# Kernel tuning notes

Measured on AMD Instinct MI355X. Metric: run time of the kernel, lower is better.

## Reference

```python
import jax, jax.numpy as jnp
import numpy as np
from jax import lax

N, CIN, COUT = 4, 3, 16
D = H = W = 64
K, S, PAD, OUT_PAD = 3, 2, 1, 1


def setup_inputs() -> dict:
    key = jax.random.key(0)
    k1, k2, k3, k4 = jax.random.split(key, 4)
    x = jax.random.normal(k1, (N, CIN, D, H, W), dtype=jnp.float32)
    # torch ConvTranspose3d weight layout: [Cin, Cout, kD, kH, kW]
    w = jax.random.normal(k2, (CIN, COUT, K, K, K), dtype=jnp.float32) * 0.1
    b = jax.random.normal(k3, (COUT,), dtype=jnp.float32) * 0.1
    subtract = jax.random.normal(k4, (COUT,), dtype=jnp.float32) * 0.1
    return {"x": x, "w": w, "b": b, "subtract": subtract}


def reference(x, w, b, subtract):
    # ConvTranspose3d(k=3, s=2, p=1, output_padding=1) as a dilated conv:
    # flip kernel spatially, swap in/out channel axes, lhs_dilation = stride,
    # padding low = k-1-p = 1, padding high = k-1-p+output_padding = 2.
    w_conv = jnp.flip(jnp.transpose(w, (1, 0, 2, 3, 4)), axis=(2, 3, 4))  # [Cout,Cin,k,k,k]
    y = lax.conv_general_dilated(
        x, w_conv,
        window_strides=(1, 1, 1),
        padding=[(1, 2), (1, 2), (1, 2)],
        lhs_dilation=(S, S, S),
        dimension_numbers=("NCDHW", "OIDHW", "NCDHW"),
    )  # [N, 16, 2D, 2H, 2W]
    y = y + b[None, :, None, None, None]
    # MaxPool3d(kernel=2, stride=2, pad=0)
    y = lax.reduce_window(
        y, -jnp.inf, lax.max,
        window_dimensions=(1, 1, 2, 2, 2),
        window_strides=(1, 1, 2, 2, 2),
        padding="VALID",
    )  # [N, 16, D, H, W]
    s = jax.nn.softmax(y, axis=1)                       # channel softmax
    z = s - subtract[None, :, None, None, None]          # per-channel subtract
    sw = z * jax.nn.sigmoid(z)                           # swish
    return jnp.max(sw, axis=1)                           # max over channels -> [N, D, H, W]
```

## Files before the change

### kernel.cpp

```cpp
#include <hip/hip_runtime.h>
#include <math.h>

#define CIN   3
#define COUT  16
#define DHW   64

__global__ __launch_bounds__(256) void fused_convt_pool_softmax_swish_max(
    const float* __restrict__ x,
    const float* __restrict__ w,
    const float* __restrict__ bias,
    const float* __restrict__ sub,
    float* __restrict__ out)
{
    const int wv = threadIdx.x;
    const int h  = blockIdx.x * blockDim.y + threadIdx.y;
    const int d  = blockIdx.y;
    const int n  = blockIdx.z;

    float xr[CIN][2][2][2];
    const size_t nbase = (size_t)n * CIN * DHW * DHW * DHW;
#pragma unroll
    for (int c = 0; c < CIN; ++c) {
#pragma unroll
        for (int dd = 0; dd < 2; ++dd) {
#pragma unroll
            for (int hh = 0; hh < 2; ++hh) {
                const int id = d + dd;
                const int ih = h + hh;
                float v = 0.0f;
                if (id < DHW && ih < DHW) {
                    v = x[nbase + (((size_t)c * DHW + id) * DHW + ih) * DHW + wv];
                }
                xr[c][dd][hh][0] = v;
                float v1 = __shfl_down(v, 1, 64);
                xr[c][dd][hh][1] = (wv == 63) ? 0.0f : v1;
            }
        }
    }

    float pooled[COUT];
#pragma unroll
    for (int co = 0; co < COUT; ++co) {
        float acc[2][2][2] = {{{0.0f,0.0f},{0.0f,0.0f}},{{0.0f,0.0f},{0.0f,0.0f}}};
#pragma unroll
        for (int c = 0; c < CIN; ++c) {
            const float* wp = w + ((size_t)c * COUT + co) * 27;
#pragma unroll
            for (int kd = 0; kd < 3; ++kd) {
                const int pd = (kd == 1) ? 0 : 1;
                const int dd = (kd == 0) ? 1 : 0;
#pragma unroll
                for (int kh = 0; kh < 3; ++kh) {
                    const int ph = (kh == 1) ? 0 : 1;
                    const int hh = (kh == 0) ? 1 : 0;
#pragma unroll
                    for (int kw = 0; kw < 3; ++kw) {
                        const int pw = (kw == 1) ? 0 : 1;
                        const int ww = (kw == 0) ? 1 : 0;
                        acc[pd][ph][pw] = fmaf(wp[kd * 9 + kh * 3 + kw],
                                               xr[c][dd][hh][ww],
                                               acc[pd][ph][pw]);
                    }
                }
            }
        }
        float mx = acc[0][0][0];
        mx = fmaxf(mx, acc[0][0][1]);
        mx = fmaxf(mx, acc[0][1][0]);
        mx = fmaxf(mx, acc[0][1][1]);
        mx = fmaxf(mx, acc[1][0][0]);
        mx = fmaxf(mx, acc[1][0][1]);
        mx = fmaxf(mx, acc[1][1][0]);
        mx = fmaxf(mx, acc[1][1][1]);
        pooled[co] = mx + bias[co];
    }

    float m = pooled[0];
#pragma unroll
    for (int co = 1; co < COUT; ++co) m = fmaxf(m, pooled[co]);
    float e[COUT];
    float s = 0.0f;
#pragma unroll
    for (int co = 0; co < COUT; ++co) {
        e[co] = __expf(pooled[co] - m);
        s += e[co];
    }
    const float inv = 1.0f / s;

    float best = -3.402823466e+38f;
#pragma unroll
    for (int co = 0; co < COUT; ++co) {
        const float z  = fmaf(e[co], inv, -sub[co]);
        const float sw = z / (1.0f + __expf(-z));
        best = fmaxf(best, sw);
    }

    out[(((size_t)n * DHW + d) * DHW + h) * DHW + wv] = best;
}

extern "C" void kernel_launch(void* const* d_in, const int* in_sizes, int n_in,
                              void* d_out, int out_size, void* d_ws, size_t ws_size,
                              hipStream_t stream) {
    const float* x   = (const float*)d_in[0];
    const float* w   = (const float*)d_in[1];
    const float* b   = (const float*)d_in[2];
    const float* sub = (const float*)d_in[3];
    float* out = (float*)d_out;

    dim3 block(64, 4, 1);
    dim3 grid(DHW / 4, DHW, 4);
    fused_convt_pool_softmax_swish_max<<<grid, block, 0, stream>>>(x, w, b, sub, out);
}
```

Measured before the change: 113.9 us.

## Compute two W outputs per thread with vectorized loads and fast reciprocals

Each thread now handles two adjacent output columns. It loads a float2 plus one neighbour from each input row in place of using a cross-lane shuffle, so every weight load is reused for twice the FMAs and the stores become float2. The block shape changes to 32x8, and launch bounds add a minimum-occupancy hint. Division in the softmax and sigmoid is replaced by hardware reciprocal approximations, which trades a little precision for fewer instructions. Register pressure roughly doubles, since there are twice as many accumulators and pooled values, which could lower occupancy or cause spills.

New measurement: 107.7 us. 5.4% less time.

```diff
diff --git a/kernel.cpp b/kernel.cpp
--- a/kernel.cpp
+++ b/kernel.cpp
@@ -5,19 +5,20 @@
 #define COUT  16
 #define DHW   64
 
-__global__ __launch_bounds__(256) void fused_convt_pool_softmax_swish_max(
+__global__ __launch_bounds__(256, 4) void fused_convt_pool_softmax_swish_max(
     const float* __restrict__ x,
     const float* __restrict__ w,
     const float* __restrict__ bias,
     const float* __restrict__ sub,
     float* __restrict__ out)
 {
-    const int wv = threadIdx.x;
+    const int tp = threadIdx.x;
     const int h  = blockIdx.x * blockDim.y + threadIdx.y;
     const int d  = blockIdx.y;
     const int n  = blockIdx.z;
+    const int w0 = tp * 2;
 
-    float xr[CIN][2][2][2];
+    float xr[CIN][2][2][3];
     const size_t nbase = (size_t)n * CIN * DHW * DHW * DHW;
 #pragma unroll
     for (int c = 0; c < CIN; ++c) {
@@ -27,24 +28,37 @@
             for (int hh = 0; hh < 2; ++hh) {
                 const int id = d + dd;
                 const int ih = h + hh;
-                float v = 0.0f;
+                float v0 = 0.0f, v1 = 0.0f, v2 = 0.0f;
                 if (id < DHW && ih < DHW) {
-                    v = x[nbase + (((size_t)c * DHW + id) * DHW + ih) * DHW + wv];
+                    const float* row = x + nbase + (((size_t)c * DHW + id) * DHW + ih) * DHW + w0;
+                    const float2 a = *(const float2*)row;
+                    v0 = a.x;
+                    v1 = a.y;
+                    if (w0 + 2 < DHW) v2 = row[2];
                 }
-                xr[c][dd][hh][0] = v;
-                float v1 = __shfl_down(v, 1, 64);
-                xr[c][dd][hh][1] = (wv == 63) ? 0.0f : v1;
+                xr[c][dd][hh][0] = v0;
+                xr[c][dd][hh][1] = v1;
+                xr[c][dd][hh][2] = v2;
             }
         }
     }
 
-    float pooled[COUT];
+    float pooled[2][COUT];
 #pragma unroll
     for (int co = 0; co < COUT; ++co) {
-        float acc[2][2][2] = {{{0.0f,0.0f},{0.0f,0.0f}},{{0.0f,0.0f},{0.0f,0.0f}}};
+        float acc[2][2][2][2];
+#pragma unroll
+        for (int v = 0; v < 2; ++v)
+#pragma unroll
+            for (int i = 0; i < 2; ++i)
+#pragma unroll
+                for (int j = 0; j < 2; ++j)
+#pragma unroll
+                    for (int k = 0; k < 2; ++k)
+                        acc[v][i][j][k] = 0.0f;
 #pragma unroll
         for (int c = 0; c < CIN; ++c) {
-            const float* wp = w + ((size_t)c * COUT + co) * 27;
+            const float* wp = w + ((size_t)(c * COUT + co)) * 27;
 #pragma unroll
             for (int kd = 0; kd < 3; ++kd) {
                 const int pd = (kd == 1) ? 0 : 1;
@@ -57,45 +71,52 @@
                     for (int kw = 0; kw < 3; ++kw) {
                         const int pw = (kw == 1) ? 0 : 1;
                         const int ww = (kw == 0) ? 1 : 0;
-                        acc[pd][ph][pw] = fmaf(wp[kd * 9 + kh * 3 + kw],
-                                               xr[c][dd][hh][ww],
-                                               acc[pd][ph][pw]);
+                        const float wt = wp[kd * 9 + kh * 3 + kw];
+#pragma unroll
+                        for (int v = 0; v < 2; ++v)
+                            acc[v][pd][ph][pw] =
+                                fmaf(wt, xr[c][dd][hh][v + ww], acc[v][pd][ph][pw]);
                     }
                 }
             }
         }
-        float mx = acc[0][0][0];
-        mx = fmaxf(mx, acc[0][0][1]);
-        mx = fmaxf(mx, acc[0][1][0]);
-        mx = fmaxf(mx, acc[0][1][1]);
-        mx = fmaxf(mx, acc[1][0][0]);
-        mx = fmaxf(mx, acc[1][0][1]);
-        mx = fmaxf(mx, acc[1][1][0]);
-        mx = fmaxf(mx, acc[1][1][1]);
-        pooled[co] = mx + bias[co];
+        const float bco = bias[co];
+#pragma unroll
+        for (int v = 0; v < 2; ++v) {
+            const float* a = &acc[v][0][0][0];
+            const float m0 = fmaxf(fmaxf(a[0], a[1]), a[2]);
+            const float m1 = fmaxf(fmaxf(a[3], a[4]), a[5]);
+            const float m2 = fmaxf(fmaxf(a[6], a[7]), m0);
+            pooled[v][co] = fmaxf(m1, m2) + bco;
+        }
     }
 
-    float m = pooled[0];
+    float res[2];
 #pragma unroll
-    for (int co = 1; co < COUT; ++co) m = fmaxf(m, pooled[co]);
-    float e[COUT];
-    float s = 0.0f;
+    for (int v = 0; v < 2; ++v) {
+        float m = pooled[v][0];
 #pragma unroll
-    for (int co = 0; co < COUT; ++co) {
-        e[co] = __expf(pooled[co] - m);
-        s += e[co];
-    }
-    const float inv = 1.0f / s;
-
-    float best = -3.402823466e+38f;
+        for (int co = 1; co < COUT; ++co) m = fmaxf(m, pooled[v][co]);
+        float e[COUT];
+        float s = 0.0f;
 #pragma unroll
-    for (int co = 0; co < COUT; ++co) {
-        const float z  = fmaf(e[co], inv, -sub[co]);
-        const float sw = z / (1.0f + __expf(-z));
-        best = fmaxf(best, sw);
+        for (int co = 0; co < COUT; ++co) {
+            e[co] = __expf(pooled[v][co] - m);
+            s += e[co];
+        }
+        const float inv = __builtin_amdgcn_rcpf(s);
+        float best = -3.402823466e+38f;
+#pragma unroll
+        for (int co = 0; co < COUT; ++co) {
+            const float z   = fmaf(e[co], inv, -sub[co]);
+            const float sig = __builtin_amdgcn_rcpf(1.0f + __expf(-z));
+            best = fmaxf(best, z * sig);
+        }
+        res[v] = best;
     }
 
-    out[(((size_t)n * DHW + d) * DHW + h) * DHW + wv] = best;
+    float* op = out + (((size_t)n * DHW + d) * DHW + h) * DHW + w0;
+    *(float2*)op = make_float2(res[0], res[1]);
 }
 
 extern "C" void kernel_launch(void* const* d_in, const int* in_sizes, int n_in,
@@ -107,7 +128,7 @@
     const float* sub = (const float*)d_in[3];
     float* out = (float*)d_out;
 
-    dim3 block(64, 4, 1);
-    dim3 grid(DHW / 4, DHW, 4);
+    dim3 block(32, 8, 1);
+    dim3 grid(DHW / 8, DHW, 4);
     fused_convt_pool_softmax_swish_max<<<grid, block, 0, stream>>>(x, w, b, sub, out);
 }
```
